# Kernel tuning notes

Measured on AMD Instinct MI355X. Metric: run time of the kernel, lower is better.

The kernel has to match this reference:

```python
import jax, jax.numpy as jnp
import numpy as np

V, E, H, D_IMG, A = 32000, 512, 512, 2048, 128
PAD_ID = 0
LN_EPS = 1e-5


def setup_inputs() -> dict:
    key = jax.random.key(0)
    ks = jax.random.split(key, 20)
    B, S, T = 32, 49, 64
    s = 0.02
    embed = jax.random.normal(ks[0], (V, E), jnp.float32) * s
    embed = embed.at[PAD_ID].set(0.0)
    return {
        "img_seq": jax.random.normal(ks[1], (B, S, D_IMG), jnp.float32),
        "tokens_in": jax.random.randint(ks[2], (B, T), 0, V, jnp.int64),
        "embed": embed,
        "W_ctx": jax.random.normal(ks[3], (E, D_IMG), jnp.float32) * s,
        "W_mix": jax.random.normal(ks[4], (E, 2 * E), jnp.float32) * s,
        "ln_g": jnp.ones((E,), jnp.float32),
        "ln_b": jnp.zeros((E,), jnp.float32),
        "W_ih": jax.random.normal(ks[5], (4 * H, E), jnp.float32) * s,
        "W_hh": jax.random.normal(ks[6], (4 * H, H), jnp.float32) * s,
        "b_ih": jnp.zeros((4 * H,), jnp.float32),
        "b_hh": jnp.zeros((4 * H,), jnp.float32),
        "W_head": jax.random.normal(ks[7], (V, H), jnp.float32) * s,
        "W_img": jax.random.normal(ks[8], (A, D_IMG), jnp.float32) * s,
        "W_hid": jax.random.normal(ks[9], (A, H), jnp.float32) * s,
        "w_score": jax.random.normal(ks[10], (A,), jnp.float32) * s,
        "W_h0": jax.random.normal(ks[11], (H, D_IMG), jnp.float32) * s,
        "b_h0": jnp.zeros((H,), jnp.float32),
        "W_c0": jax.random.normal(ks[12], (H, D_IMG), jnp.float32) * s,
        "b_c0": jnp.zeros((H,), jnp.float32),
    }


def _decode(img_seq, tokens_in, embed, W_ctx, W_mix, ln_g, ln_b,
            W_ih, W_hh, b_ih, b_hh, W_head, W_img, W_hid, w_score,
            W_h0, b_h0, W_c0, b_c0):
    # precompute image projection: [B,S,A]
    proj_image = jnp.einsum('bsd,ad->bsa', img_seq, W_img)
    g = img_seq.mean(1)  # [B, D_img]
    h = jnp.tanh(g @ W_h0.T + b_h0) * 0.5
    c = jnp.tanh(g @ W_c0.T + b_c0) * 0.5

    def step(carry, tok_t):
        h, c = carry
        emb = embed[tok_t] * (tok_t != PAD_ID)[:, None].astype(embed.dtype)
        # additive attention
        ph = h @ W_hid.T  # [B,A]
        comb = jnp.tanh(proj_image + ph[:, None, :])  # [B,S,A]
        scores = jnp.einsum('bsa,a->bs', comb, w_score)
        w = jax.nn.softmax(scores, axis=-1)
        ctx = jnp.einsum('bs,bsd->bd', w, img_seq)
        ctxE = ctx @ W_ctx.T
        x = jnp.concatenate([emb, ctxE], axis=-1) @ W_mix.T
        x = jax.nn.relu(x)
        mu = x.mean(-1, keepdims=True)
        var = ((x - mu) ** 2).mean(-1, keepdims=True)
        x = (x - mu) * jax.lax.rsqrt(var + LN_EPS) * ln_g + ln_b
        x = x + emb
        # LSTMCell (torch gate order: i, f, g, o)
        gates = x @ W_ih.T + b_ih + h @ W_hh.T + b_hh
        i_, f_, g_, o_ = jnp.split(gates, 4, axis=-1)
        c2 = jax.nn.sigmoid(f_) * c + jax.nn.sigmoid(i_) * jnp.tanh(g_)
        h2 = jax.nn.sigmoid(o_) * jnp.tanh(c2)
        logits = h2 @ W_head.T
        return (h2, c2), logits

    _, outs = jax.lax.scan(step, (h, c), tokens_in.T)  # [T,B,V]
    return jnp.transpose(outs, (1, 0, 2))  # [B,T,V]


def reference(img_seq, tokens_in, embed, W_ctx, W_mix, ln_g, ln_b,
              W_ih, W_hh, b_ih, b_hh, W_head, W_img, W_hid, w_score,
              W_h0, b_h0, W_c0, b_c0):
    return _decode(img_seq, tokens_in, embed, W_ctx, W_mix, ln_g, ln_b,
                   W_ih, W_hh, b_ih, b_hh, W_head, W_img, W_hid, w_score,
                   W_h0, b_h0, W_c0, b_c0)
```

## Files before the change

kernel.cpp:

```cpp
#include <hip/hip_runtime.h>

#define NV 32000
#define NT 64
#define NBLK 256u

typedef unsigned long long ull;
typedef unsigned short ushort;
typedef __attribute__((ext_vector_type(8))) short v8s;
typedef __attribute__((ext_vector_type(4))) float v4f;

#define WS_WBF     0
#define WS_H2BF    8192000
#define WS_IMGEM   8716288
#define WS_PROJ    9568256
#define WS_EMBM    9781248
#define WS_WHHBF   10829824
#define WS_WIHBF   11354112
#define WS_WHIDBF  11878400
#define WS_H       11911168
#define WS_XN      11943936
#define WS_C       11960320
#define WS_FLAGS   11976704
#define WS_G       11979264
#define PS_IMGBF   0
#define PS_WCTXBF  1703936
#define PS_WIMGBF  2228224
#define PS_WMIXRBF 2359296
#define PS_WMIXLBF 2490368
#define PS_IMGEBF  3342336

__device__ __forceinline__ float fsig(float x) {
    x = fminf(fmaxf(x, -30.f), 30.f);
    return 1.f / (1.f + __expf(-x));
}
__device__ __forceinline__ float ftanh(float x) {
    x = fminf(fmaxf(x, -15.f), 15.f);
    float e = __expf(2.f * x);
    return (e - 1.f) / (e + 1.f);
}
__device__ __forceinline__ unsigned short f2bf(float f) {
    union { float f; unsigned int u; } v; v.f = f;
    unsigned int u = v.u;
    return (unsigned short)((u + 0x7FFFu + ((u >> 16) & 1u)) >> 16);
}
__device__ __forceinline__ unsigned pkf(float x, float y) {
    return (unsigned)f2bf(x) | ((unsigned)f2bf(y) << 16);
}
__device__ __forceinline__ float bf_lo(unsigned u) { return __uint_as_float(u << 16); }
__device__ __forceinline__ float bf_hi(unsigned u) { return __uint_as_float(u & 0xffff0000u); }
__device__ __forceinline__ ull agld(const ull* p) {
    return __hip_atomic_load(p, __ATOMIC_RELAXED, __HIP_MEMORY_SCOPE_AGENT);
}
__device__ __forceinline__ unsigned pk2(ull v) {
    return (unsigned)f2bf(__uint_as_float((unsigned)v)) |
           ((unsigned)f2bf(__uint_as_float((unsigned)(v >> 32))) << 16);
}


__global__ __launch_bounds__(256) void k_castpad(const float* __restrict__ in,
        ushort* __restrict__ out, int R, int Rpad, int K, int ldi, int off) {
    size_t i = ((size_t)blockIdx.x * 256 + threadIdx.x) * 8;
    if (i >= (size_t)Rpad * K) return;
    int r = (int)(i / K), k = (int)(i % K);
    uint4 o = {0, 0, 0, 0};
    if (r < R) {
        const float* p = in + (size_t)r * ldi + off + k;
        float4 a = *(const float4*)(p);
        float4 b = *(const float4*)(p + 4);
        o.x = pkf(a.x, a.y); o.y = pkf(a.z, a.w);
        o.z = pkf(b.x, b.y); o.w = pkf(b.z, b.w);
    }
    *(uint4*)(out + i) = o;
}

__global__ __launch_bounds__(256) void k_castall(
        const float* __restrict__ img, const float* __restrict__ Wctx,
        const float* __restrict__ Wimg, const float* __restrict__ Wmix,
        const float* __restrict__ Whh, const float* __restrict__ Wih,
        const float* __restrict__ Whid,
        ushort* __restrict__ imgbf, ushort* __restrict__ wctxbf,
        ushort* __restrict__ wimgbf, ushort* __restrict__ wmixRbf,
        ushort* __restrict__ wmixLbf, ushort* __restrict__ whhbf,
        ushort* __restrict__ wihbf, ushort* __restrict__ whidbf,
        unsigned* __restrict__ flg) {
    int blk = blockIdx.x, tid = threadIdx.x;
    if (blk >= 3616) {
        for (int i = tid; i < 2560; i += 256) flg[i] = 0u;
        return;
    }
    const float* in; ushort* out; int R, K, ldi, off;
    if (blk < 1664)      { in = img;  out = imgbf;   R = 1568; K = 2048; ldi = 2048; off = 0; }
    else if (blk < 2176) { in = Wctx; out = wctxbf;  R = 512;  K = 2048; ldi = 2048; off = 0;   blk -= 1664; }
    else if (blk < 2304) { in = Wimg; out = wimgbf;  R = 128;  K = 2048; ldi = 2048; off = 0;   blk -= 2176; }
    else if (blk < 2432) { in = Wmix; out = wmixRbf; R = 512;  K = 512;  ldi = 1024; off = 512; blk -= 2304; }
    else if (blk < 2560) { in = Wmix; out = wmixLbf; R = 512;  K = 512;  ldi = 1024; off = 0;   blk -= 2432; }
    else if (blk < 3072) { in = Whh;  out = whhbf;   R = 2048; K = 512;  ldi = 512;  off = 0;   blk -= 2560; }
    else if (blk < 3584) { in = Wih;  out = wihbf;   R = 2048; K = 512;  ldi = 512;  off = 0;   blk -= 3072; }
    else                 { in = Whid; out = whidbf;  R = 128;  K = 512;  ldi = 512;  off = 0;   blk -= 3584; }
    size_t i = ((size_t)blk * 256 + tid) * 8;
    int r = (int)(i / K), k = (int)(i % K);
    uint4 o = {0, 0, 0, 0};
    if (r < R) {
        const float* p = in + (size_t)r * ldi + off + k;
        float4 a = *(const float4*)(p);
        float4 b = *(const float4*)(p + 4);
        o.x = pkf(a.x, a.y); o.y = pkf(a.z, a.w);
        o.z = pkf(b.x, b.y); o.w = pkf(b.z, b.w);
    }
    *(uint4*)(out + i) = o;
}

__global__ __launch_bounds__(256) void k_gemm(const ushort* __restrict__ A,
        const ushort* __restrict__ B, float* __restrict__ C, int N, int K) {
    __shared__ ushort Al[128][72];
    __shared__ ushort Bl[128][72];
    int n0 = blockIdx.x * 128, m0 = blockIdx.y * 128;
    int tid = threadIdx.x, lane = tid & 63, wid = tid >> 6;
    int wm = wid >> 1, wn = wid & 1;
    v4f acc[4][4] = {};
    for (int kt = 0; kt < K; kt += 64) {
        __syncthreads();
        #pragma unroll
        for (int i = 0; i < 4; i++) {
            int idx = i * 256 + tid;
            int row = idx >> 3, c8 = (idx & 7) * 8;
            *(uint4*)&Al[row][c8] = *(const uint4*)&A[(size_t)(m0 + row) * K + kt + c8];
            *(uint4*)&Bl[row][c8] = *(const uint4*)&B[(size_t)(n0 + row) * K + kt + c8];
        }
        __syncthreads();
        #pragma unroll
        for (int kk = 0; kk < 2; kk++) {
            v8s a[4], bfr[4];
            int ko = kk * 32 + (lane >> 4) * 8;
            #pragma unroll
            for (int mi = 0; mi < 4; mi++)
                a[mi] = *(const v8s*)&Al[wm * 64 + mi * 16 + (lane & 15)][ko];
            #pragma unroll
            for (int ni = 0; ni < 4; ni++)
                bfr[ni] = *(const v8s*)&Bl[wn * 64 + ni * 16 + (lane & 15)][ko];
            #pragma unroll
            for (int mi = 0; mi < 4; mi++)
                #pragma unroll
                for (int ni = 0; ni < 4; ni++)
                    acc[mi][ni] = __builtin_amdgcn_mfma_f32_16x16x32_bf16(a[mi], bfr[ni], acc[mi][ni], 0, 0, 0);
        }
    }
    int col = lane & 15, rbase = (lane >> 4) * 4;
    #pragma unroll
    for (int mi = 0; mi < 4; mi++)
        #pragma unroll
        for (int ni = 0; ni < 4; ni++)
            #pragma unroll
            for (int r = 0; r < 4; r++) {
                int m = m0 + wm * 64 + mi * 16 + rbase + r;
                int v = n0 + wn * 64 + ni * 16 + col;
                C[(size_t)m * N + v] = acc[mi][ni][r];
            }
}

__global__ __launch_bounds__(256) void k_gemm3(
        const ushort* __restrict__ imgbf, const ushort* __restrict__ wctxbf,
        const ushort* __restrict__ wimgbf, const float* __restrict__ embed,
        const int* __restrict__ toks, const ushort* __restrict__ wmixLbf,
        ushort* __restrict__ imgEbf, float* __restrict__ proj,
        float* __restrict__ embM) {
    __shared__ ushort Al[128][72];
    __shared__ ushort Bl[128][72];
    int bid = blockIdx.x;
    const ushort* A; const ushort* B; int mode, K, N, n0, m0;
    if (bid < 52)      { mode = 0; A = imgbf; B = wctxbf;  K = 2048; N = 512; n0 = (bid & 3) * 128; m0 = (bid >> 2) * 128; }
    else if (bid < 65) { mode = 1; A = imgbf; B = wimgbf;  K = 2048; N = 128; n0 = 0;               m0 = (bid - 52) * 128; }
    else { int e = bid - 65; mode = 2; A = nullptr; B = wmixLbf; K = 512; N = 512; n0 = (e & 3) * 128; m0 = (e >> 2) * 128; }
    int tid = threadIdx.x, lane = tid & 63, wid = tid >> 6;
    int wm = wid >> 1, wn = wid & 1;
    v4f acc[4][4] = {};
    for (int kt = 0; kt < K; kt += 64) {
        __syncthreads();
        #pragma unroll
        for (int i = 0; i < 4; i++) {
            int idx = i * 256 + tid;
            int row = idx >> 3, c8 = (idx & 7) * 8;
            if (mode == 2) {
                int rowg = m0 + row;
                int tok = toks[(rowg & 31) * 64 + (rowg >> 5)];
                uint4 oa = {0, 0, 0, 0};
                if (tok != 0) {
                    const float* pa = embed + (size_t)tok * 512 + kt + c8;
                    float4 a0 = *(const float4*)pa, a1 = *(const float4*)(pa + 4);
                    oa.x = pkf(a0.x, a0.y); oa.y = pkf(a0.z, a0.w);
                    oa.z = pkf(a1.x, a1.y); oa.w = pkf(a1.z, a1.w);
                }
                *(uint4*)&Al[row][c8] = oa;
            } else {
                *(uint4*)&Al[row][c8] = *(const uint4*)&A[(size_t)(m0 + row) * K + kt + c8];
            }
            *(uint4*)&Bl[row][c8] = *(const uint4*)&B[(size_t)(n0 + row) * K + kt + c8];
        }
        __syncthreads();
        #pragma unroll
        for (int kk = 0; kk < 2; kk++) {
            v8s a[4], bfr[4];
            int ko = kk * 32 + (lane >> 4) * 8;
            #pragma unroll
            for (int mi = 0; mi < 4; mi++)
                a[mi] = *(const v8s*)&Al[wm * 64 + mi * 16 + (lane & 15)][ko];
            #pragma unroll
            for (int ni = 0; ni < 4; ni++)
                bfr[ni] = *(const v8s*)&Bl[wn * 64 + ni * 16 + (lane & 15)][ko];
            #pragma unroll
            for (int mi = 0; mi < 4; mi++)
                #pragma unroll
                for (int ni = 0; ni < 4; ni++)
                    acc[mi][ni] = __builtin_amdgcn_mfma_f32_16x16x32_bf16(a[mi], bfr[ni], acc[mi][ni], 0, 0, 0);
        }
    }
    int col = lane & 15, rbase = (lane >> 4) * 4;
    #pragma unroll
    for (int mi = 0; mi < 4; mi++)
        #pragma unroll
        for (int ni = 0; ni < 4; ni++)
            #pragma unroll
            for (int r = 0; r < 4; r++) {
                int m = m0 + wm * 64 + mi * 16 + rbase + r;
                int v = n0 + wn * 64 + ni * 16 + col;
                if (mode == 0)      imgEbf[(size_t)m * 512 + v] = f2bf(acc[mi][ni][r]);
                else if (mode == 1) proj[(size_t)m * 128 + v] = acc[mi][ni][r];
                else                embM[(size_t)m * 512 + v] = acc[mi][ni][r];
            }
}

__global__ __launch_bounds__(256) void k_gmean(const float* __restrict__ img,
                                               float* __restrict__ g) {
    int b = blockIdx.x;
    for (int d = threadIdx.x; d < 2048; d += 256) {
        float s = 0.f;
        for (int ss = 0; ss < 49; ss++) s += img[((size_t)(b * 49 + ss)) * 2048 + d];
        g[b * 2048 + d] = s * (1.f / 49.f);
    }
}

__global__ __launch_bounds__(256) void k_h0c0(const float* __restrict__ g,
        const float* __restrict__ Wh0, const float* __restrict__ bh0,
        const float* __restrict__ Wc0, const float* __restrict__ bc0,
        float* __restrict__ h0, float* __restrict__ c0) {
    int b = blockIdx.x >> 1, m = blockIdx.x & 1;
    __shared__ float gs[2048];
    for (int d = threadIdx.x; d < 2048; d += 256) gs[d] = g[b * 2048 + d];
    __syncthreads();
    const float* W = m ? Wc0 : Wh0;
    const float* bb = m ? bc0 : bh0;
    float* out = m ? c0 : h0;
    for (int r = threadIdx.x; r < 512; r += 256) {
        float acc = 0.f;
        const float* wr = W + (size_t)r * 2048;
        for (int d = 0; d < 2048; d += 4) {
            float4 w = *(const float4*)(wr + d);
            acc += w.x * gs[d] + w.y * gs[d + 1] + w.z * gs[d + 2] + w.w * gs[d + 3];
        }
        out[b * 512 + r] = ftanh(acc + bb[r]) * 0.5f;
    }
}


__device__ __forceinline__ void waitflags(unsigned* FLG, int base, int stride,
                                          int n, unsigned tgt) {
    if (threadIdx.x < 64) {
        bool done;
        do {
            unsigned v = tgt;
            if ((int)threadIdx.x < n)
                v = __hip_atomic_load(FLG + (base + (int)threadIdx.x * stride) * 16,
                                      __ATOMIC_RELAXED, __HIP_MEMORY_SCOPE_AGENT);
            done = __all((int)(v >= tgt));
            if (!done) __builtin_amdgcn_s_sleep(1);
        } while (!done);
    }
    __syncthreads();
}

template <int SLP>
__device__ __forceinline__ void waitgates(unsigned* FLG, unsigned tgt) {
    if (threadIdx.x < 64) {
        bool done;
        do {
            unsigned v0 = __hip_atomic_load(FLG + threadIdx.x * 16,
                            __ATOMIC_RELAXED, __HIP_MEMORY_SCOPE_AGENT);
            unsigned v1 = __hip_atomic_load(FLG + (threadIdx.x + 64) * 16,
                            __ATOMIC_RELAXED, __HIP_MEMORY_SCOPE_AGENT);
            done = __all((int)(v0 >= tgt && v1 >= tgt));
            if (!done) __builtin_amdgcn_s_sleep(SLP);
        } while (!done);
    }
    __syncthreads();
}

union SMem {
    struct {
        ushort wh[64][520];
        ushort wi[64][520];
        ushort hsb[16][520];
        float gtmp[4][16][16];
        ushort h2s[16][8];
    } g;
    struct {
        float imgem[49][512];
        float projl[49][128];
        float hb[512];
        float ebs[512];
        float php[8][128];
        float ph[128];
        float scp[64][16];
        float wsm[64];
        float xps[2][512];
        float wred[8][2];
        float bc[2];
    } a;
    struct {
        ushort Al[256][72];
        ushort Bl[128][72];
    } h;
};

__device__ __forceinline__ void head_tile(SMem& sm, const ushort* __restrict__ h2bf,
        const ushort* __restrict__ Wbf, float* __restrict__ out, int m0, int n0) {
    int tid = threadIdx.x, lane = tid & 63, wid = tid >> 6;
    int wm = wid >> 1, wn = wid & 1;
    v4f acc[4][4] = {};
    for (int kt = 0; kt < 512; kt += 64) {
        __syncthreads();
        #pragma unroll
        for (int i = 0; i < 2; i++) {
            int idx = i * 1024 + tid;
            int row = idx >> 3, c8 = (idx & 7) * 8;
            const ull* p = (const ull*)&h2bf[(size_t)(m0 + row) * 512 + kt + c8];
            ull v0 = agld(p), v1 = agld(p + 1);
            *(ull*)&sm.h.Al[row][c8] = v0;
            *(ull*)&sm.h.Al[row][c8 + 4] = v1;
        }
        {
            int row = tid >> 3, c8 = (tid & 7) * 8;
            *(uint4*)&sm.h.Bl[row][c8] = *(const uint4*)&Wbf[(size_t)(n0 + row) * 512 + kt + c8];
        }
        __syncthreads();
        if (wid < 8) {
            #pragma unroll
            for (int kk = 0; kk < 2; kk++) {
                v8s a[4], bfr[4];
                int ko = kk * 32 + (lane >> 4) * 8;
                #pragma unroll
                for (int mi = 0; mi < 4; mi++)
                    a[mi] = *(const v8s*)&sm.h.Al[wm * 64 + mi * 16 + (lane & 15)][ko];
                #pragma unroll
                for (int ni = 0; ni < 4; ni++)
                    bfr[ni] = *(const v8s*)&sm.h.Bl[wn * 64 + ni * 16 + (lane & 15)][ko];
                #pragma unroll
                for (int mi = 0; mi < 4; mi++)
                    #pragma unroll
                    for (int ni = 0; ni < 4; ni++)
                        acc[mi][ni] = __builtin_amdgcn_mfma_f32_16x16x32_bf16(a[mi], bfr[ni], acc[mi][ni], 0, 0, 0);
            }
        }
    }
    if (wid < 8) {
        int col = lane & 15, rbase = (lane >> 4) * 4;
        #pragma unroll
        for (int mi = 0; mi < 4; mi++)
            #pragma unroll
            for (int ni = 0; ni < 4; ni++)
                #pragma unroll
                for (int r = 0; r < 4; r++) {
                    int m = m0 + wm * 64 + mi * 16 + rbase + r;
                    int v = n0 + wn * 64 + ni * 16 + col;
                    int b = m & 31, t = m >> 5;
                    out[((size_t)(b * 64 + t)) * 32000 + v] = acc[mi][ni][r];
                }
    }
}

__global__ __launch_bounds__(1024, 1) void k_persist(
        const int* __restrict__ toks, const float* __restrict__ embed,
        const float* __restrict__ lng, const float* __restrict__ lnb,
        const float* __restrict__ bih, const float* __restrict__ bhh,
        const float* __restrict__ wsc, const ushort* __restrict__ whidbf,
        const ushort* __restrict__ whhbf, const ushort* __restrict__ wihbf,
        const float* __restrict__ proj, const float* __restrict__ imgEM,
        const float* __restrict__ embM, float* __restrict__ H,
        const float* __restrict__ C0, float* __restrict__ XN,
        unsigned* __restrict__ FLG, ushort* __restrict__ h2bf,
        const ushort* __restrict__ Wbf, float* __restrict__ out) {
    __shared__ SMem sm;
    __shared__ unsigned sh_w;
    int blk = blockIdx.x, tid = threadIdx.x;

    if (blk < 128) {
        int jc = blk >> 2, bg = blk & 3, b0 = bg * 8;
        int wid = tid >> 6, lane = tid & 63;
        int gate = wid & 3;
        for (int i = tid; i < 4096; i += 1024) {
            int rr = i >> 6, c8 = (i & 63) * 8;
            size_t R = (size_t)((rr >> 4) * 512 + jc * 16 + (rr & 15)) * 512 + c8;
            *(uint4*)&sm.g.wh[rr][c8] = *(const uint4*)&whhbf[R];
            *(uint4*)&sm.g.wi[rr][c8] = *(const uint4*)&wihbf[R];
        }
        for (int i = tid; i < 2080; i += 1024) ((ull*)sm.g.hsb)[i] = 0;
        float c_reg = 0.f, bs0 = 0.f, bs1 = 0.f, bs2 = 0.f, bs3 = 0.f;
        if (tid < 128) {
            int jl = tid >> 3, bb = tid & 7;
            int j = jc * 16 + jl;
            c_reg = C0[(b0 + bb) * 512 + j];
            bs0 = bih[j] + bhh[j];
            bs1 = bih[512 + j] + bhh[512 + j];
            bs2 = bih[1024 + j] + bhh[1024 + j];
            bs3 = bih[1536 + j] + bhh[1536 + j];
        }
        __syncthreads();

        for (int t = 0; t < NT; t++) {
            waitflags(FLG, bg, 4, 32, (unsigned)t);
            {
                const float* Hb = H + (t & 1) * 16384 + b0 * 512;
                if (tid < 512) {
                    int bb = tid >> 6, c8 = (tid & 63) * 8;
                    const ull* p = (const ull*)(Hb + bb * 512 + c8);
                    uint4 o = { pk2(agld(p)), pk2(agld(p + 1)),
                                pk2(agld(p + 2)), pk2(agld(p + 3)) };
                    *(uint4*)&sm.g.hsb[bb][c8] = o;
                }
            }
            __syncthreads();
            v4f acc = {};
            if (wid < 4) {
                #pragma unroll
                for (int ks = 0; ks < 16; ks++) {
                    int ko = ks * 32 + (lane >> 4) * 8;
                    v8s a = *(const v8s*)&sm.g.hsb[lane & 15][ko];
                    v8s b = *(const v8s*)&sm.g.wh[gate * 16 + (lane & 15)][ko];
                    acc = __builtin_amdgcn_mfma_f32_16x16x32_bf16(a, b, acc, 0, 0, 0);
                }
            }
            waitflags(FLG, 128 + b0, 1, 8, (unsigned)(t + 1));
            {
                const float* Xb = XN + b0 * 512;
                if (tid < 512) {
                    int bb = tid >> 6, c8 = (tid & 63) * 8;
                    const ull* p = (const ull*)(Xb + bb * 512 + c8);
                    uint4 o = { pk2(agld(p)), pk2(agld(p + 1)),
                                pk2(agld(p + 2)), pk2(agld(p + 3)) };
                    *(uint4*)&sm.g.hsb[bb][c8] = o;
                }
            }
            __syncthreads();
            if (wid < 4) {
                #pragma unroll
                for (int ks = 0; ks < 16; ks++) {
                    int ko = ks * 32 + (lane >> 4) * 8;
                    v8s a = *(const v8s*)&sm.g.hsb[lane & 15][ko];
                    v8s b = *(const v8s*)&sm.g.wi[gate * 16 + (lane & 15)][ko];
                    acc = __builtin_amdgcn_mfma_f32_16x16x32_bf16(a, b, acc, 0, 0, 0);
                }
                #pragma unroll
                for (int q = 0; q < 4; q++)
                    sm.g.gtmp[gate][lane & 15][(lane >> 4) * 4 + q] = acc[q];
            }
            __syncthreads();
            if (tid < 128) {
                int jl = tid >> 3, bb = tid & 7;
                float vi = sm.g.gtmp[0][jl][bb] + bs0;
                float vf = sm.g.gtmp[1][jl][bb] + bs1;
                float vg = sm.g.gtmp[2][jl][bb] + bs2;
                float vo = sm.g.gtmp[3][jl][bb] + bs3;
                float c2 = fsig(vf) * c_reg + fsig(vi) * ftanh(vg);
                float h2 = fsig(vo) * ftanh(c2);
                c_reg = c2;
                int bglob = b0 + bb, j = jc * 16 + jl;
                __hip_atomic_store((unsigned*)&H[((t + 1) & 1) * 16384 + bglob * 512 + j],
                                   __float_as_uint(h2), __ATOMIC_RELAXED, __HIP_MEMORY_SCOPE_AGENT);
                sm.g.h2s[jl][bb] = f2bf(h2);
            }
            __syncthreads();
            if (tid < 64) {
                int jlp = tid >> 3, bb = tid & 7;
                unsigned pk = (unsigned)sm.g.h2s[2 * jlp][bb]
                            | ((unsigned)sm.g.h2s[2 * jlp + 1][bb] << 16);
                int bglob = b0 + bb, j = jc * 16 + 2 * jlp;
                __hip_atomic_store((unsigned*)&h2bf[(size_t)(t * 32 + bglob) * 512 + j],
                                   pk, __ATOMIC_RELAXED, __HIP_MEMORY_SCOPE_AGENT);
            }
            __syncthreads();
            if (tid == 0)
                __hip_atomic_store(FLG + blk * 16, (unsigned)(t + 1),
                                   __ATOMIC_RELAXED, __HIP_MEMORY_SCOPE_AGENT);
        }
    } else if (blk < 160) {
        int b = blk - 128, bgb = b >> 3;
        for (int i = tid; i < 49 * 512; i += 1024)
            sm.a.imgem[i >> 9][i & 511] = imgEM[(size_t)b * 49 * 512 + i];
        for (int i = tid; i < 49 * 128; i += 1024)
            sm.a.projl[i >> 7][i & 127] = proj[(size_t)b * 49 * 128 + i];
        __syncthreads();
        for (int t = 0; t < NT; t++) {
            waitflags(FLG, bgb, 4, 32, (unsigned)t);
            int tok = toks[b * 64 + t];
            if (tid < 256) {
                ull v = agld((const ull*)(H + (t & 1) * 16384) + b * 256 + tid);
                *(ull*)&sm.a.hb[tid * 2] = v;
            } else if (tid < 768) {
                int k = tid - 256;
                sm.a.ebs[k] = (tok == 0) ? 0.f : embed[(size_t)tok * 512 + k];
            }
            __syncthreads();
            {
                int a = tid & 127, kq = tid >> 7;
                const ushort* wr2 = whidbf + (size_t)a * 512 + kq * 64;
                const float* hp = sm.a.hb + kq * 64;
                float p = 0.f;
                #pragma unroll
                for (int k = 0; k < 64; k += 8) {
                    uint4 q = *(const uint4*)(wr2 + k);
                    float4 ha = *(const float4*)(hp + k);
                    float4 hb4 = *(const float4*)(hp + k + 4);
                    p += bf_lo(q.x)*ha.x + bf_hi(q.x)*ha.y + bf_lo(q.y)*ha.z + bf_hi(q.y)*ha.w
                       + bf_lo(q.z)*hb4.x + bf_hi(q.z)*hb4.y + bf_lo(q.w)*hb4.z + bf_hi(q.w)*hb4.w;
                }
                sm.a.php[kq][a] = p;
            }
            __syncthreads();
            if (tid < 128) {
                float p = 0.f;
                #pragma unroll
                for (int kq = 0; kq < 8; kq++) p += sm.a.php[kq][tid];
                sm.a.ph[tid] = p;
            }
            __syncthreads();
            {
                int s = tid >> 4, aq = tid & 15;
                float p = 0.f;
                if (s < 49) {
                    const float* pr = &sm.a.projl[s][aq * 8];
                    #pragma unroll
                    for (int a = 0; a < 8; a++)
                        p += ftanh(pr[a] + sm.a.ph[aq * 8 + a]) * wsc[aq * 8 + a];
                }
                sm.a.scp[s][aq] = p;
            }
            __syncthreads();
            if (tid < 64) {
                float v = 0.f;
                #pragma unroll
                for (int q = 0; q < 16; q++) v += sm.a.scp[tid][q];
                if (tid >= 49) v = -1e30f;
                float m = v;
                for (int o = 32; o > 0; o >>= 1) m = fmaxf(m, __shfl_xor(m, o));
                float e = (tid < 49) ? __expf(v - m) : 0.f;
                float su = e;
                for (int o = 32; o > 0; o >>= 1) su += __shfl_xor(su, o);
                sm.a.wsm[tid] = e / su;
            }
            __syncthreads();
            {
                int e = tid & 511, sh = tid >> 9;
                float xp = 0.f;
                if (sh == 0) xp = embM[(size_t)(t * 32 + b) * 512 + e];
                int s0 = sh * 25, s1 = sh ? 49 : 25;
                for (int s = s0; s < s1; s++)
                    xp += sm.a.wsm[s] * sm.a.imgem[s][e];
                sm.a.xps[sh][e] = xp;
            }
            __syncthreads();
            if (tid < 512) {
                float x = fmaxf(sm.a.xps[0][tid] + sm.a.xps[1][tid], 0.f);
                float s = x, s2 = x * x;
                for (int o = 32; o > 0; o >>= 1) { s += __shfl_xor(s, o); s2 += __shfl_xor(s2, o); }
                if ((tid & 63) == 0) { sm.a.wred[tid >> 6][0] = s; sm.a.wred[tid >> 6][1] = s2; }
            }
            __syncthreads();
            if (tid == 0) {
                float s = 0.f, s2 = 0.f;
                #pragma unroll
                for (int w = 0; w < 8; w++) { s += sm.a.wred[w][0]; s2 += sm.a.wred[w][1]; }
                float mu = s * (1.f / 512.f);
                float var = s2 * (1.f / 512.f) - mu * mu;
                sm.a.bc[0] = mu; sm.a.bc[1] = rsqrtf(var + 1e-5f);
            }
            __syncthreads();
            if (tid < 512) {
                float x = fmaxf(sm.a.xps[0][tid] + sm.a.xps[1][tid], 0.f);
                float xn = (x - sm.a.bc[0]) * sm.a.bc[1] * lng[tid] + lnb[tid] + sm.a.ebs[tid];
                __hip_atomic_store((unsigned*)&XN[b * 512 + tid], __float_as_uint(xn),
                                   __ATOMIC_RELAXED, __HIP_MEMORY_SCOPE_AGENT);
            }
            __syncthreads();
            if (tid == 0)
                __hip_atomic_store(FLG + (128 + b) * 16, (unsigned)(t + 1),
                                   __ATOMIC_RELAXED, __HIP_MEMORY_SCOPE_AGENT);
        }
    } else {
        int hb = blk - 160;
        unsigned have = 0;
        for (int w = hb; w < 1750; w += 96) {
            int mt = w / 250, nt = w % 250;
            unsigned need = (unsigned)(mt * 8 + 8);
            if (have < need) { waitgates<8>(FLG, need); have = need; }
            head_tile(sm, h2bf, Wbf, out, mt * 256, nt * 128);
        }
    }

    waitgates<2>(FLG, (unsigned)NT);
    for (;;) {
        if (tid == 0)
            sh_w = __hip_atomic_fetch_add(FLG + 8, 1u, __ATOMIC_RELAXED,
                                          __HIP_MEMORY_SCOPE_AGENT);
        __syncthreads();
        unsigned w = sh_w;
        __syncthreads();
        if (w >= 250u) break;
        head_tile(sm, h2bf, Wbf, out, 7 * 256, (int)w * 128);
    }
}

extern "C" void kernel_launch(void* const* d_in, const int* in_sizes, int n_in,
                              void* d_out, int out_size, void* d_ws, size_t ws_size,
                              hipStream_t stream) {
    const float* img    = (const float*)d_in[0];
    const int*   toks   = (const int*)d_in[1];
    const float* embed  = (const float*)d_in[2];
    const float* W_ctx  = (const float*)d_in[3];
    const float* W_mix  = (const float*)d_in[4];
    const float* ln_g   = (const float*)d_in[5];
    const float* ln_b   = (const float*)d_in[6];
    const float* W_ih   = (const float*)d_in[7];
    const float* W_hh   = (const float*)d_in[8];
    const float* b_ih   = (const float*)d_in[9];
    const float* b_hh   = (const float*)d_in[10];
    const float* W_head = (const float*)d_in[11];
    const float* W_img  = (const float*)d_in[12];
    const float* W_hid  = (const float*)d_in[13];
    const float* w_sc   = (const float*)d_in[14];
    const float* W_h0   = (const float*)d_in[15];
    const float* b_h0   = (const float*)d_in[16];
    const float* W_c0   = (const float*)d_in[17];
    const float* b_c0   = (const float*)d_in[18];

    float* out = (float*)d_out;
    float* ws  = (float*)d_ws;
    ushort* Wbf    = (ushort*)(ws + WS_WBF);
    ushort* h2bf   = (ushort*)(ws + WS_H2BF);
    float*  imgEM  = ws + WS_IMGEM;
    float*  proj   = ws + WS_PROJ;
    float*  embM   = ws + WS_EMBM;
    ushort* whhbf  = (ushort*)(ws + WS_WHHBF);
    ushort* wihbf  = (ushort*)(ws + WS_WIHBF);
    ushort* whidbf = (ushort*)(ws + WS_WHIDBF);
    float*  H      = ws + WS_H;
    float*  XN     = ws + WS_XN;
    float*  C      = ws + WS_C;
    unsigned* flg  = (unsigned*)(ws + WS_FLAGS);
    float*  g      = ws + WS_G;
    ushort* imgbf   = (ushort*)(ws + PS_IMGBF);
    ushort* wctxbf  = (ushort*)(ws + PS_WCTXBF);
    ushort* wimgbf  = (ushort*)(ws + PS_WIMGBF);
    ushort* wmixRbf = (ushort*)(ws + PS_WMIXRBF);
    ushort* wmixLbf = (ushort*)(ws + PS_WMIXLBF);
    ushort* imgEbf  = (ushort*)(ws + PS_IMGEBF);

    k_castall<<<3617, 256, 0, stream>>>(img, W_ctx, W_img, W_mix, W_hh, W_ih, W_hid,
                                        imgbf, wctxbf, wimgbf, wmixRbf, wmixLbf,
                                        whhbf, wihbf, whidbf, flg);
    k_gemm3<<<129, 256, 0, stream>>>(imgbf, wctxbf, wimgbf, embed, toks, wmixLbf,
                                     imgEbf, proj, embM);
    k_gemm<<<dim3(4, 13), 256, 0, stream>>>(imgEbf, wmixRbf, imgEM, 512, 512);
    k_castpad<<<8000, 256, 0, stream>>>(W_head, Wbf, 32000, 32000, 512, 512, 0);
    k_gmean<<<32, 256, 0, stream>>>(img, g);
    k_h0c0<<<64, 256, 0, stream>>>(g, W_h0, b_h0, W_c0, b_c0, H, C);

    k_persist<<<NBLK, 1024, 0, stream>>>(toks, embed, ln_g, ln_b, b_ih, b_hh, w_sc,
                                         whidbf, whhbf, wihbf, proj, imgEM, embM,
                                         H, C, XN, flg, h2bf, Wbf, out);
}
```

Measured before the change: 983.3 us.

## Fold W_head bf16 cast into idle persistent head blocks, split h0c0 grid

```diff
diff --git a/kernel.cpp b/kernel.cpp
--- a/kernel.cpp
+++ b/kernel.cpp
@@ -57,22 +57,6 @@
 }
 
 
-__global__ __launch_bounds__(256) void k_castpad(const float* __restrict__ in,
-        ushort* __restrict__ out, int R, int Rpad, int K, int ldi, int off) {
-    size_t i = ((size_t)blockIdx.x * 256 + threadIdx.x) * 8;
-    if (i >= (size_t)Rpad * K) return;
-    int r = (int)(i / K), k = (int)(i % K);
-    uint4 o = {0, 0, 0, 0};
-    if (r < R) {
-        const float* p = in + (size_t)r * ldi + off + k;
-        float4 a = *(const float4*)(p);
-        float4 b = *(const float4*)(p + 4);
-        o.x = pkf(a.x, a.y); o.y = pkf(a.z, a.w);
-        o.z = pkf(b.x, b.y); o.w = pkf(b.z, b.w);
-    }
-    *(uint4*)(out + i) = o;
-}
-
 __global__ __launch_bounds__(256) void k_castall(
         const float* __restrict__ img, const float* __restrict__ Wctx,
         const float* __restrict__ Wimg, const float* __restrict__ Wmix,
@@ -243,22 +227,21 @@
         const float* __restrict__ Wh0, const float* __restrict__ bh0,
         const float* __restrict__ Wc0, const float* __restrict__ bc0,
         float* __restrict__ h0, float* __restrict__ c0) {
-    int b = blockIdx.x >> 1, m = blockIdx.x & 1;
+    int b = blockIdx.x >> 2, m = (blockIdx.x >> 1) & 1, rh = blockIdx.x & 1;
     __shared__ float gs[2048];
     for (int d = threadIdx.x; d < 2048; d += 256) gs[d] = g[b * 2048 + d];
     __syncthreads();
     const float* W = m ? Wc0 : Wh0;
     const float* bb = m ? bc0 : bh0;
     float* out = m ? c0 : h0;
-    for (int r = threadIdx.x; r < 512; r += 256) {
-        float acc = 0.f;
-        const float* wr = W + (size_t)r * 2048;
-        for (int d = 0; d < 2048; d += 4) {
-            float4 w = *(const float4*)(wr + d);
-            acc += w.x * gs[d] + w.y * gs[d + 1] + w.z * gs[d + 2] + w.w * gs[d + 3];
-        }
-        out[b * 512 + r] = ftanh(acc + bb[r]) * 0.5f;
-    }
+    int r = rh * 256 + threadIdx.x;
+    float acc = 0.f;
+    const float* wr = W + (size_t)r * 2048;
+    for (int d = 0; d < 2048; d += 4) {
+        float4 w = *(const float4*)(wr + d);
+        acc += w.x * gs[d] + w.y * gs[d + 1] + w.z * gs[d + 2] + w.w * gs[d + 3];
+    }
+    out[b * 512 + r] = ftanh(acc + bb[r]) * 0.5f;
 }
 
 
@@ -290,6 +273,14 @@
             done = __all((int)(v0 >= tgt && v1 >= tgt));
             if (!done) __builtin_amdgcn_s_sleep(SLP);
         } while (!done);
+    }
+    __syncthreads();
+}
+
+__device__ __forceinline__ void waitcast(unsigned* FLG) {
+    if (threadIdx.x == 0) {
+        while (__hip_atomic_load(FLG + 12, __ATOMIC_RELAXED, __HIP_MEMORY_SCOPE_AGENT) < 96u)
+            __builtin_amdgcn_s_sleep(4);
     }
     __syncthreads();
 }
@@ -387,7 +378,8 @@
         const float* __restrict__ embM, float* __restrict__ H,
         const float* __restrict__ C0, float* __restrict__ XN,
         unsigned* __restrict__ FLG, ushort* __restrict__ h2bf,
-        const ushort* __restrict__ Wbf, float* __restrict__ out) {
+        const float* __restrict__ W_head, ushort* __restrict__ Wbf,
+        float* __restrict__ out) {
     __shared__ SMem sm;
     __shared__ unsigned sh_w;
     int blk = blockIdx.x, tid = threadIdx.x;
@@ -596,16 +588,31 @@
         }
     } else {
         int hb = blk - 160;
+        {
+            ull* wq = (ull*)Wbf;
+            for (size_t i = (size_t)hb * 1024 + tid; i < 4096000; i += 98304) {
+                const float* p = W_head + i * 4;
+                float4 a = *(const float4*)p;
+                ull v = (ull)pkf(a.x, a.y) | ((ull)pkf(a.z, a.w) << 32);
+                __hip_atomic_store(wq + i, v, __ATOMIC_RELAXED, __HIP_MEMORY_SCOPE_AGENT);
+            }
+            __syncthreads();
+            if (tid == 0)
+                __hip_atomic_fetch_add(FLG + 12, 1u, __ATOMIC_RELAXED,
+                                       __HIP_MEMORY_SCOPE_AGENT);
+        }
+        waitcast(FLG);
         unsigned have = 0;
         for (int w = hb; w < 1750; w += 96) {
             int mt = w / 250, nt = w % 250;
             unsigned need = (unsigned)(mt * 8 + 8);
             if (have < need) { waitgates<8>(FLG, need); have = need; }
-            head_tile(sm, h2bf, Wbf, out, mt * 256, nt * 128);
+            head_tile(sm, h2bf, (const ushort*)Wbf, out, mt * 256, nt * 128);
         }
     }
 
     waitgates<2>(FLG, (unsigned)NT);
+    waitcast(FLG);
     for (;;) {
         if (tid == 0)
             sh_w = __hip_atomic_fetch_add(FLG + 8, 1u, __ATOMIC_RELAXED,
@@ -614,7 +621,7 @@
         unsigned w = sh_w;
         __syncthreads();
         if (w >= 250u) break;
-        head_tile(sm, h2bf, Wbf, out, 7 * 256, (int)w * 128);
+        head_tile(sm, h2bf, (const ushort*)Wbf, out, 7 * 256, (int)w * 128);
     }
 }
 
@@ -669,11 +676,10 @@
     k_gemm3<<<129, 256, 0, stream>>>(imgbf, wctxbf, wimgbf, embed, toks, wmixLbf,
                                      imgEbf, proj, embM);
     k_gemm<<<dim3(4, 13), 256, 0, stream>>>(imgEbf, wmixRbf, imgEM, 512, 512);
-    k_castpad<<<8000, 256, 0, stream>>>(W_head, Wbf, 32000, 32000, 512, 512, 0);
     k_gmean<<<32, 256, 0, stream>>>(img, g);
-    k_h0c0<<<64, 256, 0, stream>>>(g, W_h0, b_h0, W_c0, b_c0, H, C);
+    k_h0c0<<<128, 256, 0, stream>>>(g, W_h0, b_h0, W_c0, b_c0, H, C);
 
     k_persist<<<NBLK, 1024, 0, stream>>>(toks, embed, ln_g, ln_b, b_ih, b_hh, w_sc,
                                          whidbf, whhbf, wihbf, proj, imgEM, embM,
-                                         H, C, XN, flg, h2bf, Wbf, out);
-}
+                                         H, C, XN, flg, h2bf, W_head, Wbf, out);
+}
```

Measured after the change: 906.7 us. 7.8% less time.
